# Kernel optimization log

Measured on AMD Instinct MI355X. Metric: run time of the kernel, lower is better.

Reference implementation:

```python
import jax, jax.numpy as jnp
import numpy as np


def setup_inputs() -> dict:
    key = jax.random.key(0)
    k1, k2 = jax.random.split(key)
    B, H, W = 64, 512, 512
    return {
        "output": jax.random.normal(k1, (B, H, W), dtype=jnp.float32),
        "target": jax.random.normal(k2, (B, H, W), dtype=jnp.float32),
        "patch_size": 8,
    }


def reference(output, target, patch_size):
    B, H, W = output.shape
    p = patch_size
    nh, nw = H // p, W // p  # torch.unfold drops any remainder
    def patches(x):
        # [B,H,W] -> [B, nh*nw, p*p], row-major over (i, j) like the nested loop
        x = x[:, : nh * p, : nw * p]
        x = x.reshape(B, nh, p, nw, p).transpose(0, 1, 3, 2, 4)
        return x.reshape(B, nh * nw, p * p)
    op = patches(output)
    tp = patches(target)
    # per-patch L1 loss (mean reduction) and per-patch mean of target
    losses = jnp.mean(jnp.abs(op - tp), axis=-1)  # [B, nh*nw]
    means = jnp.mean(tp, axis=-1)                 # [B, nh*nw]
    agree = jnp.argmax(losses, axis=-1) == jnp.argmax(means, axis=-1)  # [B]
    num_true = jnp.sum(agree).astype(jnp.int32)
    total_num = jnp.int32(B)
    num_false = total_num - num_true
    correctness = num_true.astype(jnp.float32) / total_num.astype(jnp.float32)
    return (total_num, num_true, num_false, correctness)
```

## Files before the change

### kernel.cpp

```cpp
#include <hip/hip_runtime.h>


__device__ __forceinline__ unsigned ordf(float f) {
    unsigned u = __float_as_uint(f);
    return u ^ ((u >> 31) ? 0xFFFFFFFFu : 0x80000000u);
}

__device__ __forceinline__ unsigned long long umax64(unsigned long long a,
                                                     unsigned long long b) {
    return a > b ? a : b;
}

__global__ void patch_sums_kernel(const float* __restrict__ outp,
                                  const float* __restrict__ tgt,
                                  unsigned long long* __restrict__ wsL,
                                  unsigned long long* __restrict__ wsM) {
    const int t   = threadIdx.x;
    const int wid = blockIdx.x * 4 + (t >> 6);
    const int l   = t & 63;

    const int b    = wid >> 7;
    const int rest = wid & 127;
    const int ph   = rest >> 1;
    const int h    = rest & 1;

    const size_t base = ((size_t)b * 512 + (size_t)ph * 8) * 512
                      + (size_t)h * 256 + (size_t)l * 4;
    const float* po = outp + base;
    const float* pt = tgt  + base;

    float4 o[8], g[8];
#pragma unroll
    for (int r = 0; r < 8; ++r)
        o[r] = *reinterpret_cast<const float4*>(po + (size_t)r * 512);
#pragma unroll
    for (int r = 0; r < 8; ++r)
        g[r] = *reinterpret_cast<const float4*>(pt + (size_t)r * 512);
    __builtin_amdgcn_sched_barrier(0);

    float sAbs = 0.f, sT = 0.f;
#pragma unroll
    for (int r = 0; r < 8; ++r) {
        sAbs += fabsf(o[r].x - g[r].x) + fabsf(o[r].y - g[r].y)
              + fabsf(o[r].z - g[r].z) + fabsf(o[r].w - g[r].w);
        sT   += g[r].x + g[r].y + g[r].z + g[r].w;
    }

    sAbs += __shfl_xor(sAbs, 1);
    sT   += __shfl_xor(sT, 1);

    const int idx = ph * 64 + h * 32 + (l >> 1);

    unsigned long long kl = ((unsigned long long)ordf(sAbs) << 32)
                          | (unsigned)(4095 - idx);
    unsigned long long km = ((unsigned long long)ordf(sT) << 32)
                          | (unsigned)(4095 - idx);
#pragma unroll
    for (int s = 32; s > 0; s >>= 1) {
        kl = umax64(kl, __shfl_xor(kl, s));
        km = umax64(km, __shfl_xor(km, s));
    }

    if (l == 0) { wsL[wid] = kl; wsM[wid] = km; }
}

__global__ void finalize_kernel(const unsigned long long* __restrict__ wsL,
                                const unsigned long long* __restrict__ wsM,
                                float* __restrict__ outp) {
    const int t    = threadIdx.x;
    const int q    = t >> 2;
    const int part = t & 3;

    unsigned long long ml = 0, mm = 0;
    const int base = q * 128 + part * 32;
    for (int i = 0; i < 32; ++i) {
        ml = umax64(ml, wsL[base + i]);
        mm = umax64(mm, wsM[base + i]);
    }
    ml = umax64(ml, __shfl_xor(ml, 1));
    ml = umax64(ml, __shfl_xor(ml, 2));
    mm = umax64(mm, __shfl_xor(mm, 1));
    mm = umax64(mm, __shfl_xor(mm, 2));

    __shared__ int flags[64];
    if (part == 0)
        flags[q] = ((unsigned)(ml & 0xFFFFFFFFu) == (unsigned)(mm & 0xFFFFFFFFu)) ? 1 : 0;
    __syncthreads();

    if (t < 64) {
        int v = flags[t];
#pragma unroll
        for (int s = 32; s > 0; s >>= 1) v += __shfl_down(v, s);
        if (t == 0) {
            const float nt = (float)v;
            outp[0] = 64.0f;
            outp[1] = nt;
            outp[2] = 64.0f - nt;
            outp[3] = nt / 64.0f;
        }
    }
}

extern "C" void kernel_launch(void* const* d_in, const int* in_sizes, int n_in,
                              void* d_out, int out_size, void* d_ws, size_t ws_size,
                              hipStream_t stream) {
    const float* outp = (const float*)d_in[0];
    const float* tgt  = (const float*)d_in[1];

    unsigned long long* wsL = (unsigned long long*)d_ws;
    unsigned long long* wsM = wsL + 8192;

    patch_sums_kernel<<<2048, 256, 0, stream>>>(outp, tgt, wsL, wsM);
    finalize_kernel<<<1, 256, 0, stream>>>(wsL, wsM, (float*)d_out);
}
```

Measured before the change: 30.85 us.

## Process four patch-row strips per wave with double-buffered register loads

Each wave now handles four 8-row strips of a batch image instead of one, cutting the grid from 2048 to 512 blocks. Loads for the next strip are issued into a second register buffer before the current one is reduced, so memory latency overlaps with compute. The running max is kept in registers across strips, which shrinks the cross-lane reduction and leaves fewer workspace entries for the finalize kernel to scan. The cost is higher register pressure (launch bounds allow two blocks per CU) and fewer waves in flight to hide latency.

```diff
diff --git a/kernel.cpp b/kernel.cpp
--- a/kernel.cpp
+++ b/kernel.cpp
@@ -11,57 +11,70 @@
     return a > b ? a : b;
 }
 
-__global__ void patch_sums_kernel(const float* __restrict__ outp,
-                                  const float* __restrict__ tgt,
-                                  unsigned long long* __restrict__ wsL,
-                                  unsigned long long* __restrict__ wsM) {
-    const int t   = threadIdx.x;
-    const int wid = blockIdx.x * 4 + (t >> 6);
-    const int l   = t & 63;
-
-    const int b    = wid >> 7;
-    const int rest = wid & 127;
-    const int ph   = rest >> 1;
-    const int h    = rest & 1;
-
-    const size_t base = ((size_t)b * 512 + (size_t)ph * 8) * 512
-                      + (size_t)h * 256 + (size_t)l * 4;
-    const float* po = outp + base;
-    const float* pt = tgt  + base;
-
-    float4 o[8], g[8];
+__device__ __forceinline__ void loadc(float4 (&O)[8], float4 (&G)[8],
+                                      const float* po, const float* pt) {
 #pragma unroll
     for (int r = 0; r < 8; ++r)
-        o[r] = *reinterpret_cast<const float4*>(po + (size_t)r * 512);
+        O[r] = *reinterpret_cast<const float4*>(po + (size_t)r * 512);
 #pragma unroll
     for (int r = 0; r < 8; ++r)
-        g[r] = *reinterpret_cast<const float4*>(pt + (size_t)r * 512);
-    __builtin_amdgcn_sched_barrier(0);
+        G[r] = *reinterpret_cast<const float4*>(pt + (size_t)r * 512);
+}
 
-    float sAbs = 0.f, sT = 0.f;
+__device__ __forceinline__ void consume(const float4 (&O)[8], const float4 (&G)[8],
+                                        int ws_, int l, int k,
+                                        unsigned long long& kl,
+                                        unsigned long long& km) {
+    float sA = 0.f, sT = 0.f;
 #pragma unroll
     for (int r = 0; r < 8; ++r) {
-        sAbs += fabsf(o[r].x - g[r].x) + fabsf(o[r].y - g[r].y)
-              + fabsf(o[r].z - g[r].z) + fabsf(o[r].w - g[r].w);
-        sT   += g[r].x + g[r].y + g[r].z + g[r].w;
+        sA += fabsf(O[r].x - G[r].x) + fabsf(O[r].y - G[r].y)
+            + fabsf(O[r].z - G[r].z) + fabsf(O[r].w - G[r].w);
+        sT += G[r].x + G[r].y + G[r].z + G[r].w;
     }
+    sA += __shfl_xor(sA, 1);
+    sT += __shfl_xor(sT, 1);
+    const int tb  = ws_ + 32 * k;
+    const int idx = (tb >> 1) * 64 + (tb & 1) * 32 + (l >> 1);
+    kl = umax64(kl, ((unsigned long long)ordf(sA) << 32) | (unsigned)(4095 - idx));
+    km = umax64(km, ((unsigned long long)ordf(sT) << 32) | (unsigned)(4095 - idx));
+}
 
-    sAbs += __shfl_xor(sAbs, 1);
-    sT   += __shfl_xor(sT, 1);
+__global__ __launch_bounds__(256, 2)
+void patch_kernel(const float* __restrict__ outp,
+                  const float* __restrict__ tgt,
+                  unsigned long long* __restrict__ wsL,
+                  unsigned long long* __restrict__ wsM) {
+    const int t   = threadIdx.x;
+    const int g   = blockIdx.x * 4 + (t >> 6);
+    const int l   = t & 63;
+    const int b   = g >> 5;
+    const int ws_ = g & 31;
 
-    const int idx = ph * 64 + h * 32 + (l >> 1);
+    const size_t base0 = (size_t)b * 262144 + (size_t)(ws_ >> 1) * 4096
+                       + (size_t)(ws_ & 1) * 256 + (size_t)l * 4;
+    const float* po = outp + base0;
+    const float* pt = tgt  + base0;
 
-    unsigned long long kl = ((unsigned long long)ordf(sAbs) << 32)
-                          | (unsigned)(4095 - idx);
-    unsigned long long km = ((unsigned long long)ordf(sT) << 32)
-                          | (unsigned)(4095 - idx);
+    float4 oA[8], gA[8], oB[8], gB[8];
+    unsigned long long kl = 0, km = 0;
+
+    loadc(oA, gA, po,          pt);
+    loadc(oB, gB, po + 65536,  pt + 65536);
+    consume(oA, gA, ws_, l, 0, kl, km);
+    loadc(oA, gA, po + 131072, pt + 131072);
+    consume(oB, gB, ws_, l, 1, kl, km);
+    loadc(oB, gB, po + 196608, pt + 196608);
+    consume(oA, gA, ws_, l, 2, kl, km);
+    consume(oB, gB, ws_, l, 3, kl, km);
+
 #pragma unroll
-    for (int s = 32; s > 0; s >>= 1) {
+    for (int s = 32; s > 1; s >>= 1) {
         kl = umax64(kl, __shfl_xor(kl, s));
         km = umax64(km, __shfl_xor(km, s));
     }
 
-    if (l == 0) { wsL[wid] = kl; wsM[wid] = km; }
+    if (l == 0) { wsL[g] = kl; wsM[g] = km; }
 }
 
 __global__ void finalize_kernel(const unsigned long long* __restrict__ wsL,
@@ -72,8 +85,9 @@
     const int part = t & 3;
 
     unsigned long long ml = 0, mm = 0;
-    const int base = q * 128 + part * 32;
-    for (int i = 0; i < 32; ++i) {
+    const int base = q * 32 + part * 8;
+#pragma unroll
+    for (int i = 0; i < 8; ++i) {
         ml = umax64(ml, wsL[base + i]);
         mm = umax64(mm, wsM[base + i]);
     }
@@ -84,7 +98,7 @@
 
     __shared__ int flags[64];
     if (part == 0)
-        flags[q] = ((unsigned)(ml & 0xFFFFFFFFu) == (unsigned)(mm & 0xFFFFFFFFu)) ? 1 : 0;
+        flags[q] = ((unsigned)ml == (unsigned)mm) ? 1 : 0;
     __syncthreads();
 
     if (t < 64) {
@@ -108,8 +122,8 @@
     const float* tgt  = (const float*)d_in[1];
 
     unsigned long long* wsL = (unsigned long long*)d_ws;
-    unsigned long long* wsM = wsL + 8192;
+    unsigned long long* wsM = wsL + 2048;
 
-    patch_sums_kernel<<<2048, 256, 0, stream>>>(outp, tgt, wsL, wsM);
+    patch_kernel<<<512, 256, 0, stream>>>(outp, tgt, wsL, wsM);
     finalize_kernel<<<1, 256, 0, stream>>>(wsL, wsM, (float*)d_out);
 }
```

New measurement: 26.96 us. -12.6%, faster.

## Process full patch row per wave with double-buffered chunked loads

Applied to the files above, without the earlier changes.

Each wave now covers a full 8-row patch stripe across all 512 columns, so each thread owns two patches and the grid has half as many blocks. Loads are split into four chunks with two register buffers, so computation on one chunk overlaps with loads for the next instead of issuing all loads behind a scheduling barrier. The workspace and finalize pass shrink accordingly. Fewer loads are in flight per wave at once, which may lower memory-level parallelism on this bandwidth-bound pass.

```diff
diff --git a/kernel.cpp b/kernel.cpp
--- a/kernel.cpp
+++ b/kernel.cpp
@@ -1,79 +1,95 @@
 #include <hip/hip_runtime.h>
 
+
+typedef unsigned long long u64;
 
 __device__ __forceinline__ unsigned ordf(float f) {
     unsigned u = __float_as_uint(f);
     return u ^ ((u >> 31) ? 0xFFFFFFFFu : 0x80000000u);
 }
 
-__device__ __forceinline__ unsigned long long umax64(unsigned long long a,
-                                                     unsigned long long b) {
-    return a > b ? a : b;
+__device__ __forceinline__ u64 umax64(u64 a, u64 b) { return a > b ? a : b; }
+
+__device__ __forceinline__ void loadc(float4 (&O)[4], float4 (&G)[4],
+                                      const float* po, const float* pt) {
+#pragma unroll
+    for (int j = 0; j < 4; ++j)
+        O[j] = *reinterpret_cast<const float4*>(po + (size_t)j * 256);
+#pragma unroll
+    for (int j = 0; j < 4; ++j)
+        G[j] = *reinterpret_cast<const float4*>(pt + (size_t)j * 256);
 }
 
-__global__ void patch_sums_kernel(const float* __restrict__ outp,
-                                  const float* __restrict__ tgt,
-                                  unsigned long long* __restrict__ wsL,
-                                  unsigned long long* __restrict__ wsM) {
-    const int t   = threadIdx.x;
-    const int wid = blockIdx.x * 4 + (t >> 6);
-    const int l   = t & 63;
+__device__ __forceinline__ void consume(const float4 (&O)[4], const float4 (&G)[4],
+                                        float& sA0, float& sA1,
+                                        float& sT0, float& sT1) {
+#pragma unroll
+    for (int j = 0; j < 4; ++j) {
+        const float a = fabsf(O[j].x - G[j].x) + fabsf(O[j].y - G[j].y)
+                      + fabsf(O[j].z - G[j].z) + fabsf(O[j].w - G[j].w);
+        const float m = G[j].x + G[j].y + G[j].z + G[j].w;
+        if ((j & 1) == 0) { sA0 += a; sT0 += m; }
+        else              { sA1 += a; sT1 += m; }
+    }
+}
 
-    const int b    = wid >> 7;
-    const int rest = wid & 127;
-    const int ph   = rest >> 1;
-    const int h    = rest & 1;
+__global__ void patch_kernel(const float* __restrict__ outp,
+                             const float* __restrict__ tgt,
+                             u64* __restrict__ wsL, u64* __restrict__ wsM) {
+    const int t  = threadIdx.x;
+    const int g  = blockIdx.x * 4 + (t >> 6);
+    const int l  = t & 63;
+    const int b  = g >> 6;
+    const int ph = g & 63;
 
-    const size_t base = ((size_t)b * 512 + (size_t)ph * 8) * 512
-                      + (size_t)h * 256 + (size_t)l * 4;
+    const size_t base = (size_t)b * 262144 + (size_t)ph * 4096 + (size_t)l * 4;
     const float* po = outp + base;
     const float* pt = tgt  + base;
 
-    float4 o[8], g[8];
+    float4 oA[4], gA[4], oB[4], gB[4];
+    float sA0 = 0.f, sA1 = 0.f, sT0 = 0.f, sT1 = 0.f;
+
+    loadc(oA, gA, po,        pt);
+    loadc(oB, gB, po + 1024, pt + 1024);
+    consume(oA, gA, sA0, sA1, sT0, sT1);
+    loadc(oA, gA, po + 2048, pt + 2048);
+    consume(oB, gB, sA0, sA1, sT0, sT1);
+    loadc(oB, gB, po + 3072, pt + 3072);
+    consume(oA, gA, sA0, sA1, sT0, sT1);
+    consume(oB, gB, sA0, sA1, sT0, sT1);
+
+    sA0 += __shfl_xor(sA0, 1);
+    sA1 += __shfl_xor(sA1, 1);
+    sT0 += __shfl_xor(sT0, 1);
+    sT1 += __shfl_xor(sT1, 1);
+
+    const int idx0 = ph * 64 + (l >> 1);
+    const int idx1 = ph * 64 + 32 + (l >> 1);
+
+    u64 kl = umax64(((u64)ordf(sA0) << 32) | (unsigned)(4095 - idx0),
+                    ((u64)ordf(sA1) << 32) | (unsigned)(4095 - idx1));
+    u64 km = umax64(((u64)ordf(sT0) << 32) | (unsigned)(4095 - idx0),
+                    ((u64)ordf(sT1) << 32) | (unsigned)(4095 - idx1));
+
 #pragma unroll
-    for (int r = 0; r < 8; ++r)
-        o[r] = *reinterpret_cast<const float4*>(po + (size_t)r * 512);
-#pragma unroll
-    for (int r = 0; r < 8; ++r)
-        g[r] = *reinterpret_cast<const float4*>(pt + (size_t)r * 512);
-    __builtin_amdgcn_sched_barrier(0);
-
-    float sAbs = 0.f, sT = 0.f;
-#pragma unroll
-    for (int r = 0; r < 8; ++r) {
-        sAbs += fabsf(o[r].x - g[r].x) + fabsf(o[r].y - g[r].y)
-              + fabsf(o[r].z - g[r].z) + fabsf(o[r].w - g[r].w);
-        sT   += g[r].x + g[r].y + g[r].z + g[r].w;
-    }
-
-    sAbs += __shfl_xor(sAbs, 1);
-    sT   += __shfl_xor(sT, 1);
-
-    const int idx = ph * 64 + h * 32 + (l >> 1);
-
-    unsigned long long kl = ((unsigned long long)ordf(sAbs) << 32)
-                          | (unsigned)(4095 - idx);
-    unsigned long long km = ((unsigned long long)ordf(sT) << 32)
-                          | (unsigned)(4095 - idx);
-#pragma unroll
-    for (int s = 32; s > 0; s >>= 1) {
+    for (int s = 32; s > 1; s >>= 1) {
         kl = umax64(kl, __shfl_xor(kl, s));
         km = umax64(km, __shfl_xor(km, s));
     }
-
-    if (l == 0) { wsL[wid] = kl; wsM[wid] = km; }
+    if (l == 0) { wsL[g] = kl; wsM[g] = km; }
 }
 
-__global__ void finalize_kernel(const unsigned long long* __restrict__ wsL,
-                                const unsigned long long* __restrict__ wsM,
+__global__ void finalize_kernel(const u64* __restrict__ wsL,
+                                const u64* __restrict__ wsM,
                                 float* __restrict__ outp) {
     const int t    = threadIdx.x;
     const int q    = t >> 2;
     const int part = t & 3;
 
-    unsigned long long ml = 0, mm = 0;
-    const int base = q * 128 + part * 32;
-    for (int i = 0; i < 32; ++i) {
+    u64 ml = 0, mm = 0;
+    const int base = q * 64 + part * 16;
+#pragma unroll
+    for (int i = 0; i < 16; ++i) {
         ml = umax64(ml, wsL[base + i]);
         mm = umax64(mm, wsM[base + i]);
     }
@@ -84,7 +100,7 @@
 
     __shared__ int flags[64];
     if (part == 0)
-        flags[q] = ((unsigned)(ml & 0xFFFFFFFFu) == (unsigned)(mm & 0xFFFFFFFFu)) ? 1 : 0;
+        flags[q] = ((unsigned)ml == (unsigned)mm) ? 1 : 0;
     __syncthreads();
 
     if (t < 64) {
@@ -107,9 +123,9 @@
     const float* outp = (const float*)d_in[0];
     const float* tgt  = (const float*)d_in[1];
 
-    unsigned long long* wsL = (unsigned long long*)d_ws;
-    unsigned long long* wsM = wsL + 8192;
+    u64* wsL = (u64*)d_ws;
+    u64* wsM = wsL + 4096;
 
-    patch_sums_kernel<<<2048, 256, 0, stream>>>(outp, tgt, wsL, wsM);
+    patch_kernel<<<1024, 256, 0, stream>>>(outp, tgt, wsL, wsM);
     finalize_kernel<<<1, 256, 0, stream>>>(wsL, wsM, (float*)d_out);
 }
```

Measured after the change: 33.09 us. +7.2%, slower.
